# Performance work log

Measured on AMD Instinct MI355X. Metric: run time of the kernel, lower is better.

The kernel has to match this reference:

```python
import jax, jax.numpy as jnp
import numpy as np

B, L = 16, 128
E, A = 34, 36          # num_events, num_arguments
V, D, H = 30000, 300, 256


def setup_inputs() -> dict:
    key = jax.random.key(0)
    ks = jax.random.split(key, 14)
    s = 0.08
    n = lambda k, shape: jax.random.normal(k, shape, jnp.float32) * s
    return {
        "input_ids": jax.random.randint(ks[0], (B, L), 0, V),
        "emb": n(ks[1], (V, D)),
        "Wih_f": n(ks[2], (4 * H, D)), "Whh_f": n(ks[3], (4 * H, H)),
        "bih_f": n(ks[4], (4 * H,)), "bhh_f": n(ks[5], (4 * H,)),
        "Wih_b": n(ks[6], (4 * H, D)), "Whh_b": n(ks[7], (4 * H, H)),
        "bih_b": n(ks[8], (4 * H,)), "bhh_b": n(ks[9], (4 * H,)),
        "We": n(ks[10], (E, 2 * H + E - 1)), "be": n(ks[11], (E,)),
        "Wa": n(ks[12], (A, 4 * H + A - 1 + E - 1)), "ba": n(ks[13], (A,)),
    }


def _lstm(x, Wih, Whh, bih, bhh):
    # x: [L, B, D] -> outputs [L, B, H]; PyTorch gate order i, f, g, o
    Bsz = x.shape[1]
    Hh = Whh.shape[1]
    b = bih + bhh

    def step(carry, xt):
        h, c = carry
        z = xt @ Wih.T + h @ Whh.T + b
        i, f, g, o = jnp.split(z, 4, axis=-1)
        c = jax.nn.sigmoid(f) * c + jax.nn.sigmoid(i) * jnp.tanh(g)
        h = jax.nn.sigmoid(o) * jnp.tanh(c)
        return (h, c), h

    h0 = jnp.zeros((Bsz, Hh), x.dtype)
    _, hs = jax.lax.scan(step, (h0, h0), x)
    return hs


def _forward(input_ids, emb, Wih_f, Whh_f, bih_f, bhh_f, Wih_b, Whh_b, bih_b, bhh_b, We, be, Wa, ba):
    Bsz, Ll = input_ids.shape
    x = emb[input_ids]                       # [B, L, D]
    xt = jnp.transpose(x, (1, 0, 2))         # [L, B, D]
    hf = _lstm(xt, Wih_f, Whh_f, bih_f, bhh_f)
    hb = _lstm(xt[::-1], Wih_b, Whh_b, bih_b, bhh_b)[::-1]
    hs = jnp.concatenate([hf, hb], axis=-1)  # [L, B, 2H]
    hidden = jnp.transpose(hs, (1, 0, 2))    # [B, L, 2H]

    ev_ids = jnp.arange(E - 1)
    ar_ids = jnp.arange(A - 1)
    g_trg0 = jnp.zeros((Bsz, E - 1), jnp.int32)
    g_trg_arg0 = jnp.zeros((Bsz, Ll, E - 1), jnp.int32)
    g_arg0 = jnp.zeros((Bsz, Ll, A - 1), jnp.int32)

    def step(carry, ht):                     # ht: [B, 2H] at position i
        g_trg, g_trg_arg, g_arg = carry
        ev_in = jnp.concatenate([ht, g_trg.astype(ht.dtype)], axis=1)
        ev_logit = ev_in @ We.T + be                       # [B, E]
        ev_pred = jnp.argmax(ev_logit, axis=-1)            # [B]
        trig = jnp.broadcast_to(ht[:, None, :], (Bsz, Ll, ht.shape[-1]))
        arg_in = jnp.concatenate(
            [hidden, trig, g_arg.astype(ht.dtype), g_trg_arg.astype(ht.dtype)], axis=2)
        arg_logits = arg_in @ Wa.T + ba                    # [B, L, A]
        arg_pred = jnp.argmax(arg_logits, axis=-1)         # [B, L]

        has_ev = ev_pred > 0
        # update_g_trg: g_trg[b, ev_pred[b]-1] = 1 where ev_pred>0
        g_trg = jnp.where(has_ev[:, None] & (ev_ids[None, :] == (ev_pred - 1)[:, None]), 1, g_trg)
        # update_g_trg_arg: column ev_pred-1 set to 1 where arg_pred>0
        cond_ta = (has_ev[:, None, None] & (arg_pred > 0)[:, :, None]
                   & (ev_ids[None, None, :] == (ev_pred - 1)[:, None, None]))
        g_trg_arg = jnp.where(cond_ta, 1, g_trg_arg)
        # update_g_arg: g_arg[b, j, arg_pred[b,j]-1] = 1 where ev_pred>0 and arg_pred>0
        cond_a = (has_ev[:, None, None] & (arg_pred > 0)[:, :, None]
                  & (ar_ids[None, None, :] == (arg_pred - 1)[:, :, None]))
        g_arg = jnp.where(cond_a, 1, g_arg)
        return (g_trg, g_trg_arg, g_arg), (ev_logit, arg_logits)

    _, (ev_all, arg_all) = jax.lax.scan(step, (g_trg0, g_trg_arg0, g_arg0), hs)
    event_logits = jnp.transpose(ev_all, (1, 0, 2))        # [B, L, E]
    arguments_logits = jnp.transpose(arg_all, (1, 0, 2, 3))  # [B, L, L, A]
    return event_logits, arguments_logits


def reference(input_ids, emb, Wih_f, Whh_f, bih_f, bhh_f, Wih_b, Whh_b, bih_b, bhh_b, We, be, Wa, ba):
    return _forward(input_ids, emb, Wih_f, Whh_f, bih_f, bhh_f,
                    Wih_b, Whh_b, bih_b, bhh_b, We, be, Wa, ba)
```

## Files before the change

kernel.cpp:

```cpp
#include <hip/hip_runtime.h>
#include <math.h>

#define B_  16
#define L_  128
#define E_  34
#define A_  36
#define D_  300
#define H_  256
#define DP_ 304
#define G4_ 1024
#define KC_ 512
#define NCAT_ 128
#define WAS_ 1092
#define WES_ 545

#define O_X      0u
#define O_WIHT_F 622592u
#define O_WIHT_B 933888u
#define O_HX     1245184u
#define O_BSUM_F 1769472u
#define O_BSUM_B 1770496u
#define O_ZPRE   1771520u
#define O_HIDDEN 5965824u
#define O_WCAT   7014400u
#define O_BVEC   7079936u
#define O_P      7080064u
#define O_EVTAG  7342208u

#define HIX(k) ((k) + (((k) >> 5) << 2))

#define BARRIER_LGKM() asm volatile("s_waitcnt lgkmcnt(0)\n\ts_barrier" ::: "memory")

__device__ __forceinline__ float fsig(float x) {
    return __builtin_amdgcn_rcpf(1.0f + __expf(-x));
}
__device__ __forceinline__ float ftanh(float x) {
    float e = __expf(-2.0f * fabsf(x));
    float t = (1.0f - e) * __builtin_amdgcn_rcpf(1.0f + e);
    return copysignf(t, x);
}

__global__ void k_prep(const int* __restrict__ ids, const float* __restrict__ emb,
                       const float* __restrict__ Wih_f,
                       const float* __restrict__ bih_f, const float* __restrict__ bhh_f,
                       const float* __restrict__ Wih_b,
                       const float* __restrict__ bih_b, const float* __restrict__ bhh_b,
                       const float* __restrict__ We, const float* __restrict__ be,
                       const float* __restrict__ Wa, const float* __restrict__ ba,
                       float* __restrict__ ws) {
    const int N0 = 2048 * DP_;
    const int N1 = 2 * 311296;
    const int N3 = 2 * 1024;
    const int N4 = 65536;
    const int N5 = 128;
    const int total = N0 + N1 + N3 + N4 + N5;
    for (int idx = blockIdx.x * blockDim.x + threadIdx.x; idx < total;
         idx += gridDim.x * blockDim.x) {
        int i = idx;
        if (i < N0) {
            int m = i / DP_, d = i - m * DP_;
            int t = m >> 4, b = m & 15;
            int id = ids[b * L_ + t];
            ws[O_X + i] = (d < D_) ? emb[(size_t)id * D_ + d] : 0.0f;
            continue;
        }
        i -= N0;
        if (i < N1) {
            int dir = i / 311296, rem = i % 311296;
            int k = rem >> 10, r = rem & 1023;
            const float* Wih = dir ? Wih_b : Wih_f;
            ws[(dir ? O_WIHT_B : O_WIHT_F) + rem] = (k < D_) ? Wih[r * D_ + k] : 0.0f;
            continue;
        }
        i -= N1;
        if (i < N3) {
            int dir = i / 1024, r = i % 1024;
            ws[(dir ? O_BSUM_B : O_BSUM_F) + r] =
                (dir ? bih_b[r] + bhh_b[r] : bih_f[r] + bhh_f[r]);
            continue;
        }
        i -= N3;
        if (i < N4) {
            int k = i >> 7, n = i & 127;
            float v = 0.0f;
            if (n < 36)               v = Wa[n * WAS_ + k];
            else if (n < 72)          v = Wa[(n - 36) * WAS_ + KC_ + k];
            else if (n < 106)         v = We[(n - 72) * WES_ + k];
            ws[O_WCAT + i] = v;
            continue;
        }
        i -= N4;
        {
            float v = 0.0f;
            if (i < 36)               v = ba[i];
            else if (i >= 72 && i < 106) v = be[i - 72];
            ws[O_BVEC + i] = v;
        }
    }
}

__global__ __launch_bounds__(256) void k_gemm1(float* __restrict__ ws) {
    __shared__ float As[16][64];
    __shared__ float Bs[16][64];
    int dir = blockIdx.z;
    int m0 = blockIdx.y * 64;
    int n0 = blockIdx.x * 64;
    int tid = threadIdx.x;
    const float* xp = ws + O_X;
    const float* Bt = ws + (dir ? O_WIHT_B : O_WIHT_F);
    const float* bs = ws + (dir ? O_BSUM_B : O_BSUM_F);
    float acc[4][4] = {};
    int a_m = tid >> 2, a_k = (tid & 3) << 2;
    int b_k = tid >> 4, b_n = (tid & 15) << 2;
    int ty = tid >> 4, tx = tid & 15;
    int mrow = m0 + a_m;
    int t = mrow >> 4, bb = mrow & 15;
    int srow = dir ? (((L_ - 1 - t) << 4) | bb) : mrow;
    const float* arow = xp + (size_t)srow * DP_;
    for (int k0 = 0; k0 < DP_; k0 += 16) {
        float4 av = *(const float4*)(arow + k0 + a_k);
        float4 bv = *(const float4*)(Bt + (size_t)(k0 + b_k) * G4_ + n0 + b_n);
        As[a_k + 0][a_m] = av.x; As[a_k + 1][a_m] = av.y;
        As[a_k + 2][a_m] = av.z; As[a_k + 3][a_m] = av.w;
        *(float4*)&Bs[b_k][b_n] = bv;
        __syncthreads();
#pragma unroll
        for (int kk = 0; kk < 16; kk++) {
            float4 a4 = *(const float4*)&As[kk][ty * 4];
            float4 b4 = *(const float4*)&Bs[kk][tx * 4];
            acc[0][0] = fmaf(a4.x, b4.x, acc[0][0]); acc[0][1] = fmaf(a4.x, b4.y, acc[0][1]);
            acc[0][2] = fmaf(a4.x, b4.z, acc[0][2]); acc[0][3] = fmaf(a4.x, b4.w, acc[0][3]);
            acc[1][0] = fmaf(a4.y, b4.x, acc[1][0]); acc[1][1] = fmaf(a4.y, b4.y, acc[1][1]);
            acc[1][2] = fmaf(a4.y, b4.z, acc[1][2]); acc[1][3] = fmaf(a4.y, b4.w, acc[1][3]);
            acc[2][0] = fmaf(a4.z, b4.x, acc[2][0]); acc[2][1] = fmaf(a4.z, b4.y, acc[2][1]);
            acc[2][2] = fmaf(a4.z, b4.z, acc[2][2]); acc[2][3] = fmaf(a4.z, b4.w, acc[2][3]);
            acc[3][0] = fmaf(a4.w, b4.x, acc[3][0]); acc[3][1] = fmaf(a4.w, b4.y, acc[3][1]);
            acc[3][2] = fmaf(a4.w, b4.z, acc[3][2]); acc[3][3] = fmaf(a4.w, b4.w, acc[3][3]);
        }
        __syncthreads();
    }
    float4 bias = *(const float4*)(bs + n0 + tx * 4);
    float* zp = ws + O_ZPRE + ((size_t)dir * 2048 + m0) * G4_;
#pragma unroll
    for (int i = 0; i < 4; i++) {
        float4 o;
        o.x = acc[i][0] + bias.x; o.y = acc[i][1] + bias.y;
        o.z = acc[i][2] + bias.z; o.w = acc[i][3] + bias.w;
        *(float4*)(zp + (size_t)(ty * 4 + i) * G4_ + n0 + tx * 4) = o;
    }
}

__global__ __launch_bounds__(512, 2) void k_lstm(float* __restrict__ ws,
                                                 const float* __restrict__ Whh_f,
                                                 const float* __restrict__ Whh_b) {
    int phys = blockIdx.x;
    int g    = phys >> 5;
    int cb   = phys & 31;
    int b    = cb & 15;
    int dir  = cb >> 4;
    int tid  = threadIdx.x;
    int rg   = tid >> 3;
    int kc   = tid & 7;

    const float* Whh  = dir ? Whh_b : Whh_f;
    const float* zpre = ws + O_ZPRE + (size_t)dir * 2048 * G4_;
    float* hid = ws + O_HIDDEN;
    unsigned long long* hx64 = (unsigned long long*)(ws + O_HX);

    __shared__ float h_sh[HIX(255) + 1 + 4];
    __shared__ float zbuf[256];

    int lr0  = rg << 2;
    int ggr0 = (lr0 >> 6) * 256 + g * 64 + (lr0 & 63);
    float4 w[4][8];
#pragma unroll
    for (int i = 0; i < 4; i++) {
        const float* wr = Whh + (size_t)(ggr0 + i) * H_ + (kc << 5);
#pragma unroll
        for (int c = 0; c < 8; c++) w[i][c] = *(const float4*)(wr + (c << 2));
    }
    for (int k = tid; k < HIX(255) + 1 + 4; k += 512) h_sh[k] = 0.0f;
    float c_state = 0.0f;
    float4 zv = make_float4(0.f, 0.f, 0.f, 0.f);
    if (kc == 0) zv = *(const float4*)(zpre + (size_t)(0 * B_ + b) * G4_ + ggr0);
    __syncthreads();

    for (int s = 0; s < L_; s++) {
        float4 zn = make_float4(0.f, 0.f, 0.f, 0.f);
        if (kc == 0 && s + 1 < L_)
            zn = *(const float4*)(zpre + (size_t)((s + 1) * B_ + b) * G4_ + ggr0);
        float a0 = 0.f, a1 = 0.f, a2 = 0.f, a3 = 0.f;
        const float* hp = &h_sh[kc * 36];
#pragma unroll
        for (int c = 0; c < 8; c++) {
            float4 hv = *(const float4*)(hp + (c << 2));
            a0 = fmaf(w[0][c].x, hv.x, a0); a0 = fmaf(w[0][c].y, hv.y, a0);
            a0 = fmaf(w[0][c].z, hv.z, a0); a0 = fmaf(w[0][c].w, hv.w, a0);
            a1 = fmaf(w[1][c].x, hv.x, a1); a1 = fmaf(w[1][c].y, hv.y, a1);
            a1 = fmaf(w[1][c].z, hv.z, a1); a1 = fmaf(w[1][c].w, hv.w, a1);
            a2 = fmaf(w[2][c].x, hv.x, a2); a2 = fmaf(w[2][c].y, hv.y, a2);
            a2 = fmaf(w[2][c].z, hv.z, a2); a2 = fmaf(w[2][c].w, hv.w, a2);
            a3 = fmaf(w[3][c].x, hv.x, a3); a3 = fmaf(w[3][c].y, hv.y, a3);
            a3 = fmaf(w[3][c].z, hv.z, a3); a3 = fmaf(w[3][c].w, hv.w, a3);
        }
#pragma unroll
        for (int m = 1; m < 8; m <<= 1) {
            a0 += __shfl_xor(a0, m); a1 += __shfl_xor(a1, m);
            a2 += __shfl_xor(a2, m); a3 += __shfl_xor(a3, m);
        }
        if (kc == 0) {
            float4 z4;
            z4.x = a0 + zv.x; z4.y = a1 + zv.y; z4.z = a2 + zv.z; z4.w = a3 + zv.w;
            *(float4*)&zbuf[lr0] = z4;
        }
        zv = zn;
        BARRIER_LGKM();
        int par = (s + 1) & 1;
        if (tid < 64) {
            float fi = fsig(zbuf[tid]);
            float ff = fsig(zbuf[tid + 64]);
            float gg = ftanh(zbuf[tid + 128]);
            float fo = fsig(zbuf[tid + 192]);
            c_state = ff * c_state + fi * gg;
            float h = fo * ftanh(c_state);
            int hr = g * 64 + tid;
            h_sh[HIX(hr)] = h;
            int t_orig = dir ? (L_ - 1 - s) : s;
            hid[(size_t)(t_orig * B_ + b) * KC_ + dir * H_ + hr] = h;
            if (s + 1 < L_) {
                unsigned long long pk =
                    ((unsigned long long)(unsigned)(s + 1) << 32) | (unsigned)__float_as_uint(h);
                __hip_atomic_store(&hx64[(par << 13) + (phys << 6) + tid], pk,
                                   __ATOMIC_RELAXED, __HIP_MEMORY_SCOPE_AGENT);
            }
        }
        if (tid >= 64 && tid < 256 && s + 1 < L_) {
            int which = tid >> 6;
            int sg = (g + which) & 3;
            int sb = cb | (sg << 5);
            int u  = tid & 63;
            const unsigned long long* wp = &hx64[(par << 13) + (sb << 6) + u];
            unsigned long long v;
            int cnt = 0;
            do {
                v = __hip_atomic_load(wp, __ATOMIC_RELAXED, __HIP_MEMORY_SCOPE_AGENT);
            } while ((int)(v >> 32) < s + 1 && ++cnt < (1 << 20));
            h_sh[HIX(sg * 64 + u)] = __uint_as_float((unsigned)v);
        }
        BARRIER_LGKM();
    }
}

__global__ __launch_bounds__(256) void k_gemm2(float* __restrict__ ws) {
    __shared__ float As[16][64];
    __shared__ float Bs[16][64];
    int m0 = blockIdx.y * 64;
    int n0 = blockIdx.x * 64;
    int tid = threadIdx.x;
    const float* Ap = ws + O_HIDDEN;
    const float* Bp = ws + O_WCAT;
    const float* bv = ws + O_BVEC;
    float acc[4][4] = {};
    int a_m = tid >> 2, a_k = (tid & 3) << 2;
    int b_k = tid >> 4, b_n = (tid & 15) << 2;
    int ty = tid >> 4, tx = tid & 15;
    const float* arow = Ap + (size_t)(m0 + a_m) * KC_;
    for (int k0 = 0; k0 < KC_; k0 += 16) {
        float4 av = *(const float4*)(arow + k0 + a_k);
        float4 bvv = *(const float4*)(Bp + (size_t)(k0 + b_k) * NCAT_ + n0 + b_n);
        As[a_k + 0][a_m] = av.x; As[a_k + 1][a_m] = av.y;
        As[a_k + 2][a_m] = av.z; As[a_k + 3][a_m] = av.w;
        *(float4*)&Bs[b_k][b_n] = bvv;
        __syncthreads();
#pragma unroll
        for (int kk = 0; kk < 16; kk++) {
            float4 a4 = *(const float4*)&As[kk][ty * 4];
            float4 b4 = *(const float4*)&Bs[kk][tx * 4];
            acc[0][0] = fmaf(a4.x, b4.x, acc[0][0]); acc[0][1] = fmaf(a4.x, b4.y, acc[0][1]);
            acc[0][2] = fmaf(a4.x, b4.z, acc[0][2]); acc[0][3] = fmaf(a4.x, b4.w, acc[0][3]);
            acc[1][0] = fmaf(a4.y, b4.x, acc[1][0]); acc[1][1] = fmaf(a4.y, b4.y, acc[1][1]);
            acc[1][2] = fmaf(a4.y, b4.z, acc[1][2]); acc[1][3] = fmaf(a4.y, b4.w, acc[1][3]);
            acc[2][0] = fmaf(a4.z, b4.x, acc[2][0]); acc[2][1] = fmaf(a4.z, b4.y, acc[2][1]);
            acc[2][2] = fmaf(a4.z, b4.z, acc[2][2]); acc[2][3] = fmaf(a4.z, b4.w, acc[2][3]);
            acc[3][0] = fmaf(a4.w, b4.x, acc[3][0]); acc[3][1] = fmaf(a4.w, b4.y, acc[3][1]);
            acc[3][2] = fmaf(a4.w, b4.z, acc[3][2]); acc[3][3] = fmaf(a4.w, b4.w, acc[3][3]);
        }
        __syncthreads();
    }
    float4 bias = *(const float4*)(bv + n0 + tx * 4);
    float* Pp = ws + O_P + (size_t)m0 * NCAT_;
#pragma unroll
    for (int i = 0; i < 4; i++) {
        float4 o;
        o.x = acc[i][0] + bias.x; o.y = acc[i][1] + bias.y;
        o.z = acc[i][2] + bias.z; o.w = acc[i][3] + bias.w;
        *(float4*)(Pp + (size_t)(ty * 4 + i) * NCAT_ + n0 + tx * 4) = o;
    }
}

__global__ __launch_bounds__(1024) void k_dec(const float* __restrict__ We,
                                              const float* __restrict__ Wa,
                                              float* __restrict__ ws, float* __restrict__ out) {
    const float* P = ws + O_P;
    int* evtag = (int*)(ws + O_EVTAG);
    int lane = threadIdx.x & 63;
    if (blockIdx.x == 0) {
        int b = threadIdx.x >> 6;
        float Cg = 0.0f;
        unsigned long long gmask = 0ull;
        float pv = (lane < E_) ? P[(size_t)(0 * B_ + b) * NCAT_ + 72 + lane] : 0.0f;
        float p1 = (lane < E_) ? P[(size_t)(1 * B_ + b) * NCAT_ + 72 + lane] : 0.0f;
        for (int i = 0; i < L_; i++) {
            float p2 = 0.0f;
            if (i + 2 < L_ && lane < E_) p2 = P[(size_t)((i + 2) * B_ + b) * NCAT_ + 72 + lane];
            float v = (lane < E_) ? (pv + Cg) : -INFINITY;
            float mv = v;
            int mi = (lane < E_) ? lane : 0x7fffffff;
#pragma unroll
            for (int off = 32; off; off >>= 1) {
                float ov = __shfl_down(mv, off);
                int oi = __shfl_down(mi, off);
                if (ov > mv || (ov == mv && oi < mi)) { mv = ov; mi = oi; }
            }
            int p = __shfl(mi, 0);
            if (lane == 0)
                __hip_atomic_store(&evtag[b * L_ + i], ((i + 1) << 8) | p,
                                   __ATOMIC_RELAXED, __HIP_MEMORY_SCOPE_AGENT);
            if (lane < E_) out[(size_t)(b * L_ + i) * E_ + lane] = v;
            if (p > 0) {
                unsigned long long bit = 1ull << (p - 1);
                if (!(gmask & bit)) {
                    gmask |= bit;
                    if (lane < E_) Cg += We[lane * WES_ + 2 * H_ + (p - 1)];
                }
            }
            pv = p1; p1 = p2;
        }
    } else {
        int w = ((blockIdx.x - 1) << 4) + (threadIdx.x >> 6);
        int b = w >> 7, j = w & 127;
        float* outa = out + (size_t)B_ * L_ * E_;
        float C = 0.0f;
        if (lane < A_) C = P[(size_t)(j * B_ + b) * NCAT_ + lane];
        unsigned long long ga = 0ull, gta = 0ull;
        float tv = (lane < A_) ? P[(size_t)(0 * B_ + b) * NCAT_ + 36 + lane] : 0.0f;
        float t1 = (lane < A_) ? P[(size_t)(1 * B_ + b) * NCAT_ + 36 + lane] : 0.0f;
        int myv = (int)0x80000000;
        for (int i = 0; i < L_; i++) {
            float t2 = 0.0f;
            if (i + 2 < L_ && lane < A_) t2 = P[(size_t)((i + 2) * B_ + b) * NCAT_ + 36 + lane];
            int w0 = i & ~63;
            if ((i & 63) == 0)
                myv = __hip_atomic_load(&evtag[b * L_ + w0 + lane],
                                        __ATOMIC_RELAXED, __HIP_MEMORY_SCOPE_AGENT);
            int tv_tag = __shfl(myv, i & 63);
            if ((tv_tag >> 8) < i + 1) {
                int cnt = 0;
                do {
                    __builtin_amdgcn_s_sleep(1);
                    myv = __hip_atomic_load(&evtag[b * L_ + w0 + lane],
                                            __ATOMIC_RELAXED, __HIP_MEMORY_SCOPE_AGENT);
                    tv_tag = __shfl(myv, i & 63);
                } while ((tv_tag >> 8) < i + 1 && ++cnt < (1 << 18));
            }
            int ev = tv_tag & 0xff;
            float v = (lane < A_) ? (C + tv) : -INFINITY;
            float mv = v;
            int mi = (lane < A_) ? lane : 0x7fffffff;
#pragma unroll
            for (int off = 32; off; off >>= 1) {
                float ov = __shfl_down(mv, off);
                int oi = __shfl_down(mi, off);
                if (ov > mv || (ov == mv && oi < mi)) { mv = ov; mi = oi; }
            }
            int p = __shfl(mi, 0);
            if (lane < A_) outa[(size_t)((b * L_ + i) * L_ + j) * A_ + lane] = v;
            if (ev > 0 && p > 0) {
                unsigned long long bq = 1ull << (ev - 1);
                if (!(gta & bq)) {
                    gta |= bq;
                    if (lane < A_) C += Wa[lane * WAS_ + 4 * H_ + A_ - 1 + (ev - 1)];
                }
                unsigned long long br = 1ull << (p - 1);
                if (!(ga & br)) {
                    ga |= br;
                    if (lane < A_) C += Wa[lane * WAS_ + 4 * H_ + (p - 1)];
                }
            }
            tv = t1; t1 = t2;
        }
    }
}

extern "C" void kernel_launch(void* const* d_in, const int* in_sizes, int n_in,
                              void* d_out, int out_size, void* d_ws, size_t ws_size,
                              hipStream_t stream) {
    (void)in_sizes; (void)n_in; (void)out_size; (void)ws_size;
    const int*   ids   = (const int*)d_in[0];
    const float* emb   = (const float*)d_in[1];
    const float* Wih_f = (const float*)d_in[2];
    const float* Whh_f = (const float*)d_in[3];
    const float* bih_f = (const float*)d_in[4];
    const float* bhh_f = (const float*)d_in[5];
    const float* Wih_b = (const float*)d_in[6];
    const float* Whh_b = (const float*)d_in[7];
    const float* bih_b = (const float*)d_in[8];
    const float* bhh_b = (const float*)d_in[9];
    const float* We    = (const float*)d_in[10];
    const float* be    = (const float*)d_in[11];
    const float* Wa    = (const float*)d_in[12];
    const float* ba    = (const float*)d_in[13];
    float* out = (float*)d_out;
    float* ws  = (float*)d_ws;

    hipLaunchKernelGGL(k_prep, dim3(2048), dim3(256), 0, stream,
                       ids, emb, Wih_f, bih_f, bhh_f, Wih_b, bih_b, bhh_b,
                       We, be, Wa, ba, ws);
    hipLaunchKernelGGL(k_gemm1, dim3(16, 32, 2), dim3(256), 0, stream, ws);
    hipLaunchKernelGGL(k_lstm, dim3(128), dim3(512), 0, stream, ws, Whh_f, Whh_b);
    hipLaunchKernelGGL(k_gemm2, dim3(2, 32, 1), dim3(256), 0, stream, ws);
    hipLaunchKernelGGL(k_dec, dim3(129), dim3(1024), 0, stream, We, Wa, ws, out);
}
```

Measured before the change: 524.5 us.

## Use split-bf16 MFMA for the input-projection GEMM

The input-to-hidden GEMM moves from scalar FP32 FMAs to bf16 MFMA instructions with a hi/lo split (three MFMAs per tile), which keeps close to FP32 accuracy. The prep kernel now writes the embeddings and Wih as bf16 hi/lo pairs padded to K=320, with Wih kept row-major. The GEMM tile grows to 128x128 with 4 waves. This targets the FP32 GEMM cost, at the price of extra prep work, an approximation error of the split, and uncoalesced scalar output stores.

```diff
diff --git a/kernel.cpp b/kernel.cpp
--- a/kernel.cpp
+++ b/kernel.cpp
@@ -7,29 +7,35 @@
 #define A_  36
 #define D_  300
 #define H_  256
-#define DP_ 304
+#define KP_ 320
 #define G4_ 1024
 #define KC_ 512
 #define NCAT_ 128
 #define WAS_ 1092
 #define WES_ 545
 
-#define O_X      0u
-#define O_WIHT_F 622592u
-#define O_WIHT_B 933888u
-#define O_HX     1245184u
-#define O_BSUM_F 1769472u
-#define O_BSUM_B 1770496u
-#define O_ZPRE   1771520u
-#define O_HIDDEN 5965824u
-#define O_WCAT   7014400u
-#define O_BVEC   7079936u
-#define O_P      7080064u
-#define O_EVTAG  7342208u
+#define O_XH     0u
+#define O_XL     327680u
+#define O_WH_F   655360u
+#define O_WH_B   819200u
+#define O_WL_F   983040u
+#define O_WL_B   1146880u
+#define O_HX     1310720u
+#define O_BSUM_F 1343488u
+#define O_BSUM_B 1344512u
+#define O_ZPRE   1345536u
+#define O_HIDDEN 5539840u
+#define O_WCAT   6588416u
+#define O_BVEC   6653952u
+#define O_P      6654080u
+#define O_EVTAG  6916224u
 
 #define HIX(k) ((k) + (((k) >> 5) << 2))
 
 #define BARRIER_LGKM() asm volatile("s_waitcnt lgkmcnt(0)\n\ts_barrier" ::: "memory")
+
+typedef short bf16x8 __attribute__((ext_vector_type(8)));
+typedef float f32x4  __attribute__((ext_vector_type(4)));
 
 __device__ __forceinline__ float fsig(float x) {
     return __builtin_amdgcn_rcpf(1.0f + __expf(-x));
@@ -38,6 +44,13 @@
     float e = __expf(-2.0f * fabsf(x));
     float t = (1.0f - e) * __builtin_amdgcn_rcpf(1.0f + e);
     return copysignf(t, x);
+}
+__device__ __forceinline__ unsigned short f2bf(float f) {
+    unsigned u = __float_as_uint(f);
+    return (unsigned short)((u + 0x7fffu + ((u >> 16) & 1u)) >> 16);
+}
+__device__ __forceinline__ float bf2f(unsigned short h) {
+    return __uint_as_float(((unsigned)h) << 16);
 }
 
 __global__ void k_prep(const int* __restrict__ ids, const float* __restrict__ emb,
@@ -48,28 +61,38 @@
                        const float* __restrict__ We, const float* __restrict__ be,
                        const float* __restrict__ Wa, const float* __restrict__ ba,
                        float* __restrict__ ws) {
-    const int N0 = 2048 * DP_;
-    const int N1 = 2 * 311296;
+    const int N0 = 2048 * KP_;
+    const int N1 = 2 * G4_ * KP_;
     const int N3 = 2 * 1024;
     const int N4 = 65536;
     const int N5 = 128;
     const int total = N0 + N1 + N3 + N4 + N5;
+    unsigned short* xh = (unsigned short*)(ws + O_XH);
+    unsigned short* xl = (unsigned short*)(ws + O_XL);
     for (int idx = blockIdx.x * blockDim.x + threadIdx.x; idx < total;
          idx += gridDim.x * blockDim.x) {
         int i = idx;
         if (i < N0) {
-            int m = i / DP_, d = i - m * DP_;
+            int m = i / KP_, d = i - m * KP_;
             int t = m >> 4, b = m & 15;
             int id = ids[b * L_ + t];
-            ws[O_X + i] = (d < D_) ? emb[(size_t)id * D_ + d] : 0.0f;
+            float f = (d < D_) ? emb[(size_t)id * D_ + d] : 0.0f;
+            unsigned short h = f2bf(f);
+            xh[i] = h;
+            xl[i] = f2bf(f - bf2f(h));
             continue;
         }
         i -= N0;
         if (i < N1) {
-            int dir = i / 311296, rem = i % 311296;
-            int k = rem >> 10, r = rem & 1023;
+            int dir = i / (G4_ * KP_), rem = i % (G4_ * KP_);
+            int r = rem / KP_, k = rem - r * KP_;
             const float* Wih = dir ? Wih_b : Wih_f;
-            ws[(dir ? O_WIHT_B : O_WIHT_F) + rem] = (k < D_) ? Wih[r * D_ + k] : 0.0f;
+            unsigned short* wh = (unsigned short*)(ws + (dir ? O_WH_B : O_WH_F));
+            unsigned short* wl = (unsigned short*)(ws + (dir ? O_WL_B : O_WL_F));
+            float f = (k < D_) ? Wih[r * D_ + k] : 0.0f;
+            unsigned short h = f2bf(f);
+            wh[rem] = h;
+            wl[rem] = f2bf(f - bf2f(h));
             continue;
         }
         i -= N1;
@@ -100,53 +123,90 @@
 }
 
 __global__ __launch_bounds__(256) void k_gemm1(float* __restrict__ ws) {
-    __shared__ float As[16][64];
-    __shared__ float Bs[16][64];
+    __shared__ unsigned short Ah[128][40];
+    __shared__ unsigned short Al[128][40];
+    __shared__ unsigned short Bh[128][40];
+    __shared__ unsigned short Bl[128][40];
     int dir = blockIdx.z;
-    int m0 = blockIdx.y * 64;
-    int n0 = blockIdx.x * 64;
+    int m0 = blockIdx.y * 128;
+    int n0 = blockIdx.x * 128;
     int tid = threadIdx.x;
-    const float* xp = ws + O_X;
-    const float* Bt = ws + (dir ? O_WIHT_B : O_WIHT_F);
-    const float* bs = ws + (dir ? O_BSUM_B : O_BSUM_F);
-    float acc[4][4] = {};
-    int a_m = tid >> 2, a_k = (tid & 3) << 2;
-    int b_k = tid >> 4, b_n = (tid & 15) << 2;
-    int ty = tid >> 4, tx = tid & 15;
-    int mrow = m0 + a_m;
-    int t = mrow >> 4, bb = mrow & 15;
-    int srow = dir ? (((L_ - 1 - t) << 4) | bb) : mrow;
-    const float* arow = xp + (size_t)srow * DP_;
-    for (int k0 = 0; k0 < DP_; k0 += 16) {
-        float4 av = *(const float4*)(arow + k0 + a_k);
-        float4 bv = *(const float4*)(Bt + (size_t)(k0 + b_k) * G4_ + n0 + b_n);
-        As[a_k + 0][a_m] = av.x; As[a_k + 1][a_m] = av.y;
-        As[a_k + 2][a_m] = av.z; As[a_k + 3][a_m] = av.w;
-        *(float4*)&Bs[b_k][b_n] = bv;
+    const unsigned short* xh = (const unsigned short*)(ws + O_XH);
+    const unsigned short* xl = (const unsigned short*)(ws + O_XL);
+    const unsigned short* wh = (const unsigned short*)(ws + (dir ? O_WH_B : O_WH_F));
+    const unsigned short* wl = (const unsigned short*)(ws + (dir ? O_WL_B : O_WL_F));
+    const float* bsv = ws + (dir ? O_BSUM_B : O_BSUM_F);
+
+    int w = tid >> 6, lane = tid & 63;
+    int wr = w >> 1, wc = w & 1;
+    int lr = lane & 15, lk = lane >> 4;
+
+    int sr = tid >> 1, sh = tid & 1;
+    int gm = m0 + sr;
+    int tt = gm >> 4, bb2 = gm & 15;
+    int srow = dir ? (((L_ - 1 - tt) << 4) | bb2) : gm;
+    size_t aoff = (size_t)srow * KP_ + sh * 16;
+    size_t boff = (size_t)(n0 + sr) * KP_ + sh * 16;
+    int swb = sr * 80 + sh * 32;
+
+    f32x4 acc[4][4] = {};
+    for (int k0 = 0; k0 < KP_; k0 += 32) {
+        float4 vah0 = *(const float4*)(xh + aoff + k0);
+        float4 vah1 = *(const float4*)(xh + aoff + k0 + 8);
+        float4 val0 = *(const float4*)(xl + aoff + k0);
+        float4 val1 = *(const float4*)(xl + aoff + k0 + 8);
+        float4 vbh0 = *(const float4*)(wh + boff + k0);
+        float4 vbh1 = *(const float4*)(wh + boff + k0 + 8);
+        float4 vbl0 = *(const float4*)(wl + boff + k0);
+        float4 vbl1 = *(const float4*)(wl + boff + k0 + 8);
+        *(float4*)((char*)&Ah[0][0] + swb) = vah0;
+        *(float4*)((char*)&Ah[0][0] + swb + 16) = vah1;
+        *(float4*)((char*)&Al[0][0] + swb) = val0;
+        *(float4*)((char*)&Al[0][0] + swb + 16) = val1;
+        *(float4*)((char*)&Bh[0][0] + swb) = vbh0;
+        *(float4*)((char*)&Bh[0][0] + swb + 16) = vbh1;
+        *(float4*)((char*)&Bl[0][0] + swb) = vbl0;
+        *(float4*)((char*)&Bl[0][0] + swb + 16) = vbl1;
         __syncthreads();
-#pragma unroll
-        for (int kk = 0; kk < 16; kk++) {
-            float4 a4 = *(const float4*)&As[kk][ty * 4];
-            float4 b4 = *(const float4*)&Bs[kk][tx * 4];
-            acc[0][0] = fmaf(a4.x, b4.x, acc[0][0]); acc[0][1] = fmaf(a4.x, b4.y, acc[0][1]);
-            acc[0][2] = fmaf(a4.x, b4.z, acc[0][2]); acc[0][3] = fmaf(a4.x, b4.w, acc[0][3]);
-            acc[1][0] = fmaf(a4.y, b4.x, acc[1][0]); acc[1][1] = fmaf(a4.y, b4.y, acc[1][1]);
-            acc[1][2] = fmaf(a4.y, b4.z, acc[1][2]); acc[1][3] = fmaf(a4.y, b4.w, acc[1][3]);
-            acc[2][0] = fmaf(a4.z, b4.x, acc[2][0]); acc[2][1] = fmaf(a4.z, b4.y, acc[2][1]);
-            acc[2][2] = fmaf(a4.z, b4.z, acc[2][2]); acc[2][3] = fmaf(a4.z, b4.w, acc[2][3]);
-            acc[3][0] = fmaf(a4.w, b4.x, acc[3][0]); acc[3][1] = fmaf(a4.w, b4.y, acc[3][1]);
-            acc[3][2] = fmaf(a4.w, b4.z, acc[3][2]); acc[3][3] = fmaf(a4.w, b4.w, acc[3][3]);
-        }
+        bf16x8 afh[4], afl[4], bfh[4], bfl[4];
+#pragma unroll
+        for (int mi = 0; mi < 4; mi++) {
+            int rb = (wr * 64 + mi * 16 + lr) * 80 + lk * 16;
+            afh[mi] = *(const bf16x8*)((const char*)&Ah[0][0] + rb);
+            afl[mi] = *(const bf16x8*)((const char*)&Al[0][0] + rb);
+        }
+#pragma unroll
+        for (int ni = 0; ni < 4; ni++) {
+            int rb = (wc * 64 + ni * 16 + lr) * 80 + lk * 16;
+            bfh[ni] = *(const bf16x8*)((const char*)&Bh[0][0] + rb);
+            bfl[ni] = *(const bf16x8*)((const char*)&Bl[0][0] + rb);
+        }
+#pragma unroll
+        for (int mi = 0; mi < 4; mi++)
+#pragma unroll
+            for (int ni = 0; ni < 4; ni++) {
+                acc[mi][ni] = __builtin_amdgcn_mfma_f32_16x16x32_bf16(
+                    afh[mi], bfh[ni], acc[mi][ni], 0, 0, 0);
+                acc[mi][ni] = __builtin_amdgcn_mfma_f32_16x16x32_bf16(
+                    afh[mi], bfl[ni], acc[mi][ni], 0, 0, 0);
+                acc[mi][ni] = __builtin_amdgcn_mfma_f32_16x16x32_bf16(
+                    afl[mi], bfh[ni], acc[mi][ni], 0, 0, 0);
+            }
         __syncthreads();
     }
-    float4 bias = *(const float4*)(bs + n0 + tx * 4);
-    float* zp = ws + O_ZPRE + ((size_t)dir * 2048 + m0) * G4_;
-#pragma unroll
-    for (int i = 0; i < 4; i++) {
-        float4 o;
-        o.x = acc[i][0] + bias.x; o.y = acc[i][1] + bias.y;
-        o.z = acc[i][2] + bias.z; o.w = acc[i][3] + bias.w;
-        *(float4*)(zp + (size_t)(ty * 4 + i) * G4_ + n0 + tx * 4) = o;
+    float* zp = ws + O_ZPRE + (size_t)dir * 2048 * G4_;
+    int crow = (lane >> 4) * 4;
+#pragma unroll
+    for (int ni = 0; ni < 4; ni++) {
+        int n = n0 + wc * 64 + ni * 16 + lr;
+        float bias = bsv[n];
+#pragma unroll
+        for (int mi = 0; mi < 4; mi++) {
+            int mb = m0 + wr * 64 + mi * 16 + crow;
+#pragma unroll
+            for (int j = 0; j < 4; j++)
+                zp[(size_t)(mb + j) * G4_ + n] = acc[mi][ni][j] + bias;
+        }
     }
 }
 
@@ -201,7 +261,7 @@
             a2 = fmaf(w[2][c].x, hv.x, a2); a2 = fmaf(w[2][c].y, hv.y, a2);
             a2 = fmaf(w[2][c].z, hv.z, a2); a2 = fmaf(w[2][c].w, hv.w, a2);
             a3 = fmaf(w[3][c].x, hv.x, a3); a3 = fmaf(w[3][c].y, hv.y, a3);
-            a3 = fmaf(w[3][c].z, hv.z, a3); a3 = fmaf(w[3][c].w, hv.w, a3);
+            a3 = fmaf(w[3][c].w, hv.w, a3); a3 = fmaf(w[3][c].z, hv.z, a3);
         }
 #pragma unroll
         for (int m = 1; m < 8; m <<= 1) {
@@ -416,7 +476,7 @@
     hipLaunchKernelGGL(k_prep, dim3(2048), dim3(256), 0, stream,
                        ids, emb, Wih_f, bih_f, bhh_f, Wih_b, bih_b, bhh_b,
                        We, be, Wa, ba, ws);
-    hipLaunchKernelGGL(k_gemm1, dim3(16, 32, 2), dim3(256), 0, stream, ws);
+    hipLaunchKernelGGL(k_gemm1, dim3(8, 16, 2), dim3(256), 0, stream, ws);
     hipLaunchKernelGGL(k_lstm, dim3(128), dim3(512), 0, stream, ws, Whh_f, Whh_b);
     hipLaunchKernelGGL(k_gemm2, dim3(2, 32, 1), dim3(256), 0, stream, ws);
     hipLaunchKernelGGL(k_dec, dim3(129), dim3(1024), 0, stream, We, Wa, ws, out);
```

Measured after the change: 520.2 us. Within noise of the previous version (-0.8%).
